# Performance work log

Hardware: AMD Instinct MI355X
Metric: run time of the kernel (lower is better)

## Reference

```python
import jax, jax.numpy as jnp
import numpy as np

N_, E_, A_, B_, H_, DH_ = 8000, 12000, 48000, 64, 64, 4096
STEPS, POOL_ITERS = 4, 3

def rbf(x, K, cutoff):
    mu = jnp.linspace(0.0, cutoff, K).astype(x.dtype)
    gamma = 1.0 / (cutoff / (K - 1)) ** 2
    return jnp.exp(-gamma * (x[..., None] - mu) ** 2)

def gru_step(x, h, Wih, Whh, bih, bhh):
    gi = x @ Wih.T + bih
    gh = h @ Whh.T + bhh
    ir, iz, inew = jnp.split(gi, 3, axis=-1)
    hr, hz, hnew = jnp.split(gh, 3, axis=-1)
    r = jax.nn.sigmoid(ir + hr)
    z = jax.nn.sigmoid(iz + hz)
    n = jnp.tanh(inew + r * hnew)
    return (1.0 - z) * n + z * h

def lstm_step(x, h, c, Wih, Whh, bih, bhh):
    g = x @ Wih.T + bih + h @ Whh.T + bhh
    i, f, gg, o = jnp.split(g, 4, axis=-1)
    c2 = jax.nn.sigmoid(f) * c + jax.nn.sigmoid(i) * jnp.tanh(gg)
    h2 = jax.nn.sigmoid(o) * jnp.tanh(c2)
    return h2, c2

def seg_softmax(e, seg, num_seg):
    m = jax.ops.segment_max(e, seg, num_segments=num_seg)
    ex = jnp.exp(e - m[seg])
    s = jax.ops.segment_sum(ex, seg, num_segments=num_seg)
    return ex / s[seg]

def _forward(node_attribute, edge_attribute, edge_length, angle, edge_src, edge_dst, angle_src, angle_dst, graph_ids, projW, projb, bondW, bondb, efW, efb, gnn_b, buW, bub, auW, aub, gWih, gWhh, gbih, gbhh, sWih0, sWhh0, sbih0, sbhh0, sWih1, sWhh1, sbih1, sbhh1, spW, spb, prelu_a):
    N, E = node_attribute.shape[0], edge_src.shape[0]
    x0 = jax.nn.relu(node_attribute @ projW + projb)  # [N, H]
    len_rbf = rbf(edge_length, 8, 4.0)                # [E, 8]
    edge_feat = jnp.concatenate([edge_attribute, len_rbf], axis=-1)  # [E, 16]
    ee_feat = jnp.concatenate([rbf(angle, 8, float(np.pi)), len_rbf[angle_src]], axis=-1)  # [A, 16]
    Wb = (edge_feat @ bondW + bondb).reshape(E, H_, H_)  # per-bond weight matrices (constant over steps)
    Wa = (ee_feat @ efW + efb).reshape(-1, H_, H_)       # per-angle weight matrices
    nf, hid = x0, x0
    for _ in range(STEPS):
        bm = nf[edge_src]                                # gather src node feats per bond [E, H]
        ha = jax.nn.relu(bm @ auW + aub)                 # angle_update
        m_ang = jnp.einsum('ai,aio->ao', ha[angle_src], Wa)  # [A, H]
        amsg = jax.ops.segment_sum(m_ang, angle_dst, num_segments=E)  # scatter-sum to bonds
        hb = jax.nn.relu(bm @ buW + bub) + amsg          # bond_update + angle message
        m = jnp.einsum('ei,eio->eo', hb, Wb)             # [E, H]
        nf = jax.nn.relu(jax.ops.segment_sum(m, edge_dst, num_segments=N) + gnn_b)
        nf = gru_step(nf, hid, gWih, gWhh, gbih, gbhh)   # 1-step, 1-layer GRU: output == new hidden
        hid = nf
    agg = jnp.concatenate([nf, x0], axis=-1)             # [N, 2H]
    D = agg.shape[-1]
    q_star = jnp.zeros((B_, 2 * D), agg.dtype)
    h0 = jnp.zeros((B_, D), agg.dtype); c0 = h0
    h1 = h0; c1 = h0
    for _ in range(POOL_ITERS):                          # Set2Set
        h0, c0 = lstm_step(q_star, h0, c0, sWih0, sWhh0, sbih0, sbhh0)
        h1, c1 = lstm_step(h0, h1, c1, sWih1, sWhh1, sbih1, sbhh1)
        q = h1                                           # [B, D]
        e = jnp.sum(agg * q[graph_ids], axis=-1)         # [N]
        alpha = seg_softmax(e, graph_ids, B_)
        readout = jax.ops.segment_sum(alpha[:, None] * agg, graph_ids, num_segments=B_)
        q_star = jnp.concatenate([q, readout], axis=-1)  # [B, 2D]
    out = q_star @ spW + spb                             # [B, DH]
    return jnp.where(out >= 0, out, prelu_a * out)       # PReLU

def setup_inputs():
    key = jax.random.key(0)
    ks = jax.random.split(key, 40)
    r = lambda i, shape, s=1.0: s * jax.random.normal(ks[i], shape, jnp.float32)
    inp = {}
    inp['node_attribute'] = r(0, (N_, 110))
    inp['edge_attribute'] = r(1, (E_, 8))
    inp['edge_length'] = jax.random.uniform(ks[2], (E_,), jnp.float32, 0.5, 4.0)
    inp['angle'] = jax.random.uniform(ks[3], (A_,), jnp.float32, 0.0, float(np.pi))
    inp['edge_src'] = jax.random.randint(ks[4], (E_,), 0, N_)
    inp['edge_dst'] = jax.random.randint(ks[5], (E_,), 0, N_)
    inp['angle_src'] = jax.random.randint(ks[6], (A_,), 0, E_)
    inp['angle_dst'] = jax.random.randint(ks[7], (A_,), 0, E_)
    inp['graph_ids'] = jnp.sort(jax.random.randint(ks[8], (N_,), 0, B_))
    w = 0.05
    inp['projW'] = r(9, (110, H_), w); inp['projb'] = jnp.zeros((H_,), jnp.float32)
    inp['bondW'] = r(10, (16, H_ * H_), w); inp['bondb'] = jnp.zeros((H_ * H_,), jnp.float32)
    inp['efW'] = r(11, (16, H_ * H_), w); inp['efb'] = jnp.zeros((H_ * H_,), jnp.float32)
    inp['gnn_b'] = jnp.zeros((H_,), jnp.float32)
    inp['buW'] = r(12, (H_, H_), w); inp['bub'] = jnp.zeros((H_,), jnp.float32)
    inp['auW'] = r(13, (H_, H_), w); inp['aub'] = jnp.zeros((H_,), jnp.float32)
    inp['gWih'] = r(14, (3 * H_, H_), w); inp['gWhh'] = r(15, (3 * H_, H_), w)
    inp['gbih'] = jnp.zeros((3 * H_,), jnp.float32); inp['gbhh'] = jnp.zeros((3 * H_,), jnp.float32)
    D = 2 * H_  # Set2Set feature dim = 128
    inp['sWih0'] = r(16, (4 * D, 2 * D), w); inp['sWhh0'] = r(17, (4 * D, D), w)
    inp['sbih0'] = jnp.zeros((4 * D,), jnp.float32); inp['sbhh0'] = jnp.zeros((4 * D,), jnp.float32)
    inp['sWih1'] = r(18, (4 * D, D), w); inp['sWhh1'] = r(19, (4 * D, D), w)
    inp['sbih1'] = jnp.zeros((4 * D,), jnp.float32); inp['sbhh1'] = jnp.zeros((4 * D,), jnp.float32)
    inp['spW'] = r(20, (4 * H_, DH_), w); inp['spb'] = jnp.zeros((DH_,), jnp.float32)
    inp['prelu_a'] = jnp.full((1,), 0.25, jnp.float32)
    return inp

def reference(node_attribute, edge_attribute, edge_length, angle, edge_src, edge_dst, angle_src, angle_dst, graph_ids, projW, projb, bondW, bondb, efW, efb, gnn_b, buW, bub, auW, aub, gWih, gWhh, gbih, gbhh, sWih0, sWhh0, sbih0, sbhh0, sWih1, sWhh1, sbih1, sbhh1, spW, spb, prelu_a):
    return _forward(node_attribute, edge_attribute, edge_length, angle, edge_src, edge_dst, angle_src, angle_dst, graph_ids, projW, projb, bondW, bondb, efW, efb, gnn_b, buW, bub, auW, aub, gWih, gWhh, gbih, gbhh, sWih0, sWhh0, sbih0, sbhh0, sWih1, sWhh1, sbih1, sbhh1, spW, spb, prelu_a)
```

## Files before the change

kernel.cpp:

```cpp
#include <hip/hip_runtime.h>
#include <math.h>

#define N_N 8000
#define N_E 12000
#define N_A 48000
#define N_B 64
#define N_H 64
#define N_DH 4096

typedef _Float16 h16;
typedef __attribute__((ext_vector_type(8))) _Float16 h16x8;
typedef __attribute__((ext_vector_type(4))) float f32x4;

__device__ __forceinline__ float atomAddF(float* p, float v) {
  return __hip_atomic_fetch_add(p, v, __ATOMIC_RELAXED, __HIP_MEMORY_SCOPE_AGENT);
}
__device__ __forceinline__ float sigm(float x) { return 1.f / (1.f + expf(-x)); }


__global__ void k_proj(const float* __restrict__ na, const float* __restrict__ W,
                       const float* __restrict__ b, float* __restrict__ x0) {
  int wid = (blockIdx.x * blockDim.x + threadIdx.x) >> 6;
  int lane = threadIdx.x & 63;
  if (wid >= N_N) return;
  const float* row = na + (size_t)wid * 110;
  float acc = b[lane];
  for (int k = 0; k < 110; ++k) acc = fmaf(row[k], W[k * 64 + lane], acc);
  x0[(size_t)wid * 64 + lane] = fmaxf(acc, 0.f);
}

__global__ void k_feat(const float* __restrict__ ea, const float* __restrict__ el,
                       const float* __restrict__ ang, const int* __restrict__ asrc,
                       float* __restrict__ ef, float* __restrict__ ee) {
  int i = blockIdx.x * blockDim.x + threadIdx.x;
  const float g2 = (7.f / 4.f) * (7.f / 4.f);
  if (i < N_E) {
    int e = i;
    float x = el[e];
#pragma unroll
    for (int j = 0; j < 8; ++j) ef[e * 16 + j] = ea[e * 8 + j];
#pragma unroll
    for (int j = 0; j < 8; ++j) {
      float d = x - j * (4.f / 7.f);
      ef[e * 16 + 8 + j] = expf(-g2 * d * d);
    }
  } else if (i < N_E + N_A) {
    int a = i - N_E;
    const float PIf = 3.14159265358979323846f;
    float x = ang[a];
    float g1 = (7.f / PIf) * (7.f / PIf);
#pragma unroll
    for (int j = 0; j < 8; ++j) {
      float d = x - j * (PIf / 7.f);
      ee[a * 16 + j] = expf(-g1 * d * d);
    }
    float y = el[asrc[a]];
#pragma unroll
    for (int j = 0; j < 8; ++j) {
      float d = y - j * (4.f / 7.f);
      ee[a * 16 + 8 + j] = expf(-g2 * d * d);
    }
  }
}

#define PREP_B0 32768
#define PREP_B1 (PREP_B0 + 69632)
#define PREP_B2 (PREP_B1 + 69632)
#define PREP_B3 (PREP_B2 + 4096)
#define PREP_B4 (PREP_B3 + 4096)
__global__ void k_prep(const float* __restrict__ gWih, const float* __restrict__ gWhh,
                       const float* __restrict__ efW, const float* __restrict__ efb,
                       const float* __restrict__ bondW, const float* __restrict__ bondb,
                       const float* __restrict__ auW, const float* __restrict__ buW,
                       h16* __restrict__ W3t, h16* __restrict__ ttA,
                       h16* __restrict__ ttB, h16* __restrict__ wtAU,
                       h16* __restrict__ wtBU) {
  int i = blockIdx.x * blockDim.x + threadIdx.x;
  if (i < PREP_B0) {
    int col = i >> 7, k = i & 127;
    int grp = col >> 6, u = col & 63;
    float v;
    if (grp == 0) v = (k < 64) ? gWih[u * 64 + k] : gWhh[u * 64 + k - 64];
    else if (grp == 1) v = (k < 64) ? gWih[(64 + u) * 64 + k] : gWhh[(64 + u) * 64 + k - 64];
    else if (grp == 2) v = (k < 64) ? gWih[(128 + u) * 64 + k] : 0.f;
    else v = (k < 64) ? 0.f : gWhh[(128 + u) * 64 + k - 64];
    W3t[i] = (h16)v;
  } else if (i < PREP_B1) {
    int j = i - PREP_B0;
    int n = j >> 6, i2 = j & 63;
    int k = n >> 6, o = n & 63;
    float val = (k < 16) ? efW[(size_t)k * 4096 + i2 * 64 + o] : efb[i2 * 64 + o];
    ttA[j] = (h16)val;
  } else if (i < PREP_B2) {
    int j = i - PREP_B1;
    int n = j >> 6, i2 = j & 63;
    int k = n >> 6, o = n & 63;
    float val = (k < 16) ? bondW[(size_t)k * 4096 + i2 * 64 + o] : bondb[i2 * 64 + o];
    ttB[j] = (h16)val;
  } else if (i < PREP_B3) {
    int j = i - PREP_B2;
    int o = j >> 6, i2 = j & 63;
    wtAU[j] = (h16)auW[i2 * 64 + o];
  } else if (i < PREP_B4) {
    int j = i - PREP_B3;
    int o = j >> 6, i2 = j & 63;
    wtBU[j] = (h16)buW[i2 * 64 + o];
  }
}

__global__ void k_bounds2(const int* __restrict__ gid, int* __restrict__ gstart,
                          int* __restrict__ gend) {
  int n = blockIdx.x * blockDim.x + threadIdx.x;
  if (n >= N_N) return;
  int g = gid[n];
  if (n == 0 || gid[n - 1] != g) gstart[g] = n;
  if (n == N_N - 1 || gid[n + 1] != g) gend[g] = n + 1;
}


template <bool ADD_AMSG>
__global__ __launch_bounds__(256) void k_mfma_mlp(
    const float* __restrict__ v, const int* __restrict__ src,
    const h16* __restrict__ Wt, const float* __restrict__ bias,
    const float* __restrict__ amsg, h16* __restrict__ out, int T,
    float4* __restrict__ zbuf, int zcount4) {
  if (blockIdx.y == 0 && zbuf) {
    int stride = gridDim.x * 256;
    for (int i = blockIdx.x * 256 + threadIdx.x; i < zcount4; i += stride)
      zbuf[i] = (float4){0.f, 0.f, 0.f, 0.f};
  }
  int tid = threadIdx.x, wave = tid >> 6, lane = tid & 63;
  int l15 = lane & 15, lq = lane >> 4;
  int oc = blockIdx.y;
  int ib0 = blockIdx.x * 128 + wave * 32;

  h16x8 afr[2][2];
#pragma unroll
  for (int s = 0; s < 2; ++s) {
    int item = ib0 + s * 16 + l15;
    if (item >= T) item = T - 1;
    const float* vp = v + (size_t)src[item] * 64;
#pragma unroll
    for (int ks = 0; ks < 2; ++ks) {
      const float4* p = (const float4*)(vp + ks * 32 + 8 * lq);
      float4 x0 = p[0], x1 = p[1];
      h16x8 a;
      a[0] = (h16)x0.x; a[1] = (h16)x0.y; a[2] = (h16)x0.z; a[3] = (h16)x0.w;
      a[4] = (h16)x1.x; a[5] = (h16)x1.y; a[6] = (h16)x1.z; a[7] = (h16)x1.w;
      afr[s][ks] = a;
    }
  }
  h16x8 bfr[2][2];
#pragma unroll
  for (int nt = 0; nt < 2; ++nt)
#pragma unroll
    for (int ks = 0; ks < 2; ++ks)
      bfr[nt][ks] = *(const h16x8*)(Wt + (size_t)((oc * 2 + nt) * 16 + l15) * 64 +
                                    ks * 32 + 8 * lq);

  f32x4 acc[2][2];
#pragma unroll
  for (int s = 0; s < 2; ++s)
#pragma unroll
    for (int nt = 0; nt < 2; ++nt) acc[s][nt] = (f32x4){0.f, 0.f, 0.f, 0.f};
#pragma unroll
  for (int s = 0; s < 2; ++s)
#pragma unroll
    for (int nt = 0; nt < 2; ++nt)
#pragma unroll
      for (int ks = 0; ks < 2; ++ks)
        acc[s][nt] = __builtin_amdgcn_mfma_f32_16x16x32_f16(afr[s][ks], bfr[nt][ks],
                                                            acc[s][nt], 0, 0, 0);
#pragma unroll
  for (int s = 0; s < 2; ++s) {
#pragma unroll
    for (int nt = 0; nt < 2; ++nt) {
      int o = (oc * 2 + nt) * 16 + l15;
      float bo = bias[o];
#pragma unroll
      for (int r = 0; r < 4; ++r) {
        int item = ib0 + s * 16 + lq * 4 + r;
        if (item < T) {
          float val = fmaxf(acc[s][nt][r] + bo, 0.f);
          if (ADD_AMSG) val += amsg[(size_t)item * 64 + o];
          out[(size_t)item * 64 + o] = (h16)val;
        }
      }
    }
  }
}

template <bool GATHER>
__global__ __launch_bounds__(256) void k_mfma_mm(
    const h16* __restrict__ v, const int* __restrict__ src,
    const float* __restrict__ feat, const h16* __restrict__ Tt,
    const int* __restrict__ dst, float* __restrict__ out, int T) {
  __shared__ float f_lds[128 * 17];
  __shared__ int dst_lds[128];
  int tid = threadIdx.x;
  int base = blockIdx.x * 128;
  int oc = blockIdx.y;
  for (int e = tid; e < 128 * 16; e += 256) {
    int il = e >> 4, k = e & 15;
    int g = base + il;
    if (g >= T) g = T - 1;
    f_lds[il * 17 + k] = feat[(size_t)g * 16 + k];
  }
  if (tid < 128) {
    int g = base + tid;
    if (g >= T) g = T - 1;
    dst_lds[tid] = dst[g];
  }
  __syncthreads();

  int wave = tid >> 6, lane = tid & 63;
  int l15 = lane & 15, lq = lane >> 4;
  int ibl = wave * 32;
  int ib0 = base + ibl;

  h16x8 afr[2][2];
#pragma unroll
  for (int s = 0; s < 2; ++s) {
    int item = ib0 + s * 16 + l15;
    if (item >= T) item = T - 1;
    int vi = GATHER ? src[item] : item;
    const h16* vp = v + (size_t)vi * 64;
#pragma unroll
    for (int ks = 0; ks < 2; ++ks)
      afr[s][ks] = *(const h16x8*)(vp + ks * 32 + 8 * lq);
  }

  f32x4 acc[2][2];
#pragma unroll
  for (int s = 0; s < 2; ++s)
#pragma unroll
    for (int nt = 0; nt < 2; ++nt) acc[s][nt] = (f32x4){0.f, 0.f, 0.f, 0.f};

  for (int kk = 0; kk < 16; ++kk) {
    h16x8 bfr[2][2];
#pragma unroll
    for (int nt = 0; nt < 2; ++nt)
#pragma unroll
      for (int ks = 0; ks < 2; ++ks)
        bfr[nt][ks] = *(const h16x8*)(Tt + (size_t)(kk * 64 + (oc * 2 + nt) * 16 + l15) * 64 +
                                      ks * 32 + 8 * lq);
    h16x8 a2[2][2];
#pragma unroll
    for (int s = 0; s < 2; ++s) {
      h16 fs = (h16)f_lds[(ibl + s * 16 + l15) * 17 + kk];
      a2[s][0] = afr[s][0] * fs;
      a2[s][1] = afr[s][1] * fs;
    }
#pragma unroll
    for (int s = 0; s < 2; ++s)
#pragma unroll
      for (int nt = 0; nt < 2; ++nt)
#pragma unroll
        for (int ks = 0; ks < 2; ++ks)
          acc[s][nt] = __builtin_amdgcn_mfma_f32_16x16x32_f16(a2[s][ks], bfr[nt][ks],
                                                              acc[s][nt], 0, 0, 0);
  }
  {
    h16x8 bfr[2][2];
#pragma unroll
    for (int nt = 0; nt < 2; ++nt)
#pragma unroll
      for (int ks = 0; ks < 2; ++ks)
        bfr[nt][ks] = *(const h16x8*)(Tt + (size_t)(16 * 64 + (oc * 2 + nt) * 16 + l15) * 64 +
                                      ks * 32 + 8 * lq);
#pragma unroll
    for (int s = 0; s < 2; ++s)
#pragma unroll
      for (int nt = 0; nt < 2; ++nt)
#pragma unroll
        for (int ks = 0; ks < 2; ++ks)
          acc[s][nt] = __builtin_amdgcn_mfma_f32_16x16x32_f16(afr[s][ks], bfr[nt][ks],
                                                              acc[s][nt], 0, 0, 0);
  }

#pragma unroll
  for (int s = 0; s < 2; ++s) {
#pragma unroll
    for (int r = 0; r < 4; ++r) {
      int il = ibl + s * 16 + lq * 4 + r;
      int item = base + il;
      if (item < T) {
        float* op = out + (size_t)dst_lds[il] * 64;
#pragma unroll
        for (int nt = 0; nt < 2; ++nt)
          atomAddF(op + (oc * 2 + nt) * 16 + l15, acc[s][nt][r]);
      }
    }
  }
}

__global__ __launch_bounds__(256) void k_gru2(
    const float* __restrict__ nacc, const float* __restrict__ gnnb,
    const float* __restrict__ h, const h16* __restrict__ W3t,
    const float* __restrict__ gbih, const float* __restrict__ gbhh,
    float* __restrict__ hout, const float* __restrict__ x0,
    float* __restrict__ agg, int wagg) {
  int tid = threadIdx.x, wave = tid >> 6, lane = tid & 63;
  int l15 = lane & 15, lq = lane >> 4;
  int ib0 = blockIdx.x * 64 + wave * 16;
  int nodeA = ib0 + l15;
  if (nodeA >= N_N) nodeA = N_N - 1;

  h16x8 afr[4];
#pragma unroll
  for (int ks = 0; ks < 2; ++ks) {
    const float4* p = (const float4*)(nacc + (size_t)nodeA * 64 + ks * 32 + 8 * lq);
    const float4* gp = (const float4*)(gnnb + ks * 32 + 8 * lq);
    float4 v0 = p[0], v1 = p[1], g0 = gp[0], g1 = gp[1];
    h16x8 a;
    a[0] = (h16)fmaxf(v0.x + g0.x, 0.f); a[1] = (h16)fmaxf(v0.y + g0.y, 0.f);
    a[2] = (h16)fmaxf(v0.z + g0.z, 0.f); a[3] = (h16)fmaxf(v0.w + g0.w, 0.f);
    a[4] = (h16)fmaxf(v1.x + g1.x, 0.f); a[5] = (h16)fmaxf(v1.y + g1.y, 0.f);
    a[6] = (h16)fmaxf(v1.z + g1.z, 0.f); a[7] = (h16)fmaxf(v1.w + g1.w, 0.f);
    afr[ks] = a;
  }
#pragma unroll
  for (int ks = 0; ks < 2; ++ks) {
    const float4* p = (const float4*)(h + (size_t)nodeA * 64 + ks * 32 + 8 * lq);
    float4 v0 = p[0], v1 = p[1];
    h16x8 a;
    a[0] = (h16)v0.x; a[1] = (h16)v0.y; a[2] = (h16)v0.z; a[3] = (h16)v0.w;
    a[4] = (h16)v1.x; a[5] = (h16)v1.y; a[6] = (h16)v1.z; a[7] = (h16)v1.w;
    afr[2 + ks] = a;
  }

  f32x4 acc[16];
#pragma unroll
  for (int nt = 0; nt < 16; ++nt) acc[nt] = (f32x4){0.f, 0.f, 0.f, 0.f};
#pragma unroll
  for (int nt = 0; nt < 16; ++nt) {
#pragma unroll
    for (int ks = 0; ks < 4; ++ks) {
      if (nt >= 8 && nt < 12 && ks >= 2) continue;
      if (nt >= 12 && ks < 2) continue;
      h16x8 b = *(const h16x8*)(W3t + (size_t)(nt * 16 + l15) * 128 + ks * 32 + 8 * lq);
      acc[nt] = __builtin_amdgcn_mfma_f32_16x16x32_f16(afr[ks], b, acc[nt], 0, 0, 0);
    }
  }

#pragma unroll
  for (int nt0 = 0; nt0 < 4; ++nt0) {
    int u = nt0 * 16 + l15;
    float br = gbih[u] + gbhh[u];
    float bz = gbih[64 + u] + gbhh[64 + u];
    float bin_ = gbih[128 + u];
    float bhn = gbhh[128 + u];
#pragma unroll
    for (int r = 0; r < 4; ++r) {
      int node = ib0 + lq * 4 + r;
      if (node < N_N) {
        float rr = sigm(acc[nt0][r] + br);
        float zz = sigm(acc[nt0 + 4][r] + bz);
        float nn = tanhf(acc[nt0 + 8][r] + bin_ + rr * (acc[nt0 + 12][r] + bhn));
        float hv = h[(size_t)node * 64 + u];
        float val = (1.f - zz) * nn + zz * hv;
        hout[(size_t)node * 64 + u] = val;
        if (wagg) {
          agg[(size_t)node * 128 + u] = val;
          agg[(size_t)node * 128 + 64 + u] = x0[(size_t)node * 64 + u];
        }
      }
    }
  }
}


__global__ __launch_bounds__(256) void k_lstm2(
    const float* __restrict__ x, int xdim,
    const float* __restrict__ hin, const float* __restrict__ cin,
    const float* __restrict__ Wih, const float* __restrict__ Whh,
    const float* __restrict__ bih, const float* __restrict__ bhh,
    float* __restrict__ hout, float* __restrict__ cout) {
  int w = (blockIdx.x * blockDim.x + threadIdx.x) >> 6;
  int lane = threadIdx.x & 63;
  if (w >= N_B * 128) return;
  int b = w >> 7, u = w & 127;
  float a0 = 0.f, a1 = 0.f, a2 = 0.f, a3 = 0.f;
  const float* xr = x + (size_t)b * xdim;
  for (int k = lane; k < xdim; k += 64) {
    float xv = xr[k];
    a0 = fmaf(xv, Wih[(size_t)u * xdim + k], a0);
    a1 = fmaf(xv, Wih[(size_t)(128 + u) * xdim + k], a1);
    a2 = fmaf(xv, Wih[(size_t)(256 + u) * xdim + k], a2);
    a3 = fmaf(xv, Wih[(size_t)(384 + u) * xdim + k], a3);
  }
  const float* hr = hin + (size_t)b * 128;
#pragma unroll
  for (int k0 = 0; k0 < 128; k0 += 64) {
    int k = k0 + lane;
    float hv = hr[k];
    a0 = fmaf(hv, Whh[(size_t)u * 128 + k], a0);
    a1 = fmaf(hv, Whh[(size_t)(128 + u) * 128 + k], a1);
    a2 = fmaf(hv, Whh[(size_t)(256 + u) * 128 + k], a2);
    a3 = fmaf(hv, Whh[(size_t)(384 + u) * 128 + k], a3);
  }
#pragma unroll
  for (int m = 1; m < 64; m <<= 1) {
    a0 += __shfl_xor(a0, m);
    a1 += __shfl_xor(a1, m);
    a2 += __shfl_xor(a2, m);
    a3 += __shfl_xor(a3, m);
  }
  if (lane == 0) {
    float gi = a0 + bih[u] + bhh[u];
    float gf = a1 + bih[128 + u] + bhh[128 + u];
    float gg = a2 + bih[256 + u] + bhh[256 + u];
    float go = a3 + bih[384 + u] + bhh[384 + u];
    float c2 = sigm(gf) * cin[(size_t)b * 128 + u] + sigm(gi) * tanhf(gg);
    hout[(size_t)b * 128 + u] = sigm(go) * tanhf(c2);
    cout[(size_t)b * 128 + u] = c2;
  }
}

__global__ __launch_bounds__(256) void k_pool2(
    const float* __restrict__ agg, const int* __restrict__ gstart,
    const int* __restrict__ gend, const float* __restrict__ q,
    float* __restrict__ q_star) {
  int g = blockIdx.x;
  int s = gstart[g], t = gend[g];
  int cnt = t - s;
  if (cnt < 0) cnt = 0;
  if (cnt > 1024) cnt = 1024;
  __shared__ float ew[1024];
  __shared__ float red[8];
  __shared__ float comb[256];
  int tid = threadIdx.x, wave = tid >> 6, lane = tid & 63;
  float qa = q[g * 128 + lane], qb = q[g * 128 + 64 + lane];
  for (int i = wave; i < cnt; i += 4) {
    int n = s + i;
    float a = agg[(size_t)n * 128 + lane] * qa + agg[(size_t)n * 128 + 64 + lane] * qb;
#pragma unroll
    for (int m = 1; m < 64; m <<= 1) a += __shfl_xor(a, m);
    if (lane == 0) ew[i] = a;
  }
  __syncthreads();
  float mx = -INFINITY;
  for (int i = tid; i < cnt; i += 256) mx = fmaxf(mx, ew[i]);
#pragma unroll
  for (int m = 1; m < 64; m <<= 1) mx = fmaxf(mx, __shfl_xor(mx, m));
  if (lane == 0) red[wave] = mx;
  __syncthreads();
  mx = fmaxf(fmaxf(red[0], red[1]), fmaxf(red[2], red[3]));
  float sm = 0.f;
  for (int i = tid; i < cnt; i += 256) sm += expf(ew[i] - mx);
#pragma unroll
  for (int m = 1; m < 64; m <<= 1) sm += __shfl_xor(sm, m);
  if (lane == 0) red[4 + wave] = sm;
  __syncthreads();
  sm = red[4] + red[5] + red[6] + red[7];
  float inv = (sm > 0.f) ? 1.f / sm : 0.f;
  __syncthreads();
  for (int i = tid; i < cnt; i += 256) ew[i] = expf(ew[i] - mx) * inv;
  __syncthreads();
  int d = tid & 127, half = tid >> 7;
  float acc = 0.f;
  for (int i = half; i < cnt; i += 2)
    acc = fmaf(ew[i], agg[(size_t)(s + i) * 128 + d], acc);
  comb[tid] = acc;
  __syncthreads();
  if (half == 0) {
    float r2 = acc + comb[128 + tid];
    q_star[(size_t)g * 256 + d] = q[(size_t)g * 128 + d];
    q_star[(size_t)g * 256 + 128 + d] = r2;
  }
}

__global__ void k_out(const float* __restrict__ qs, const float* __restrict__ W,
                      const float* __restrict__ bias, const float* __restrict__ pa,
                      float* __restrict__ out) {
  int idx = blockIdx.x * blockDim.x + threadIdx.x;
  if (idx >= N_B * N_DH) return;
  int b = idx >> 12, d = idx & 4095;
  float acc = bias[d];
  const float* q = qs + (size_t)b * 256;
  for (int k = 0; k < 256; ++k) acc = fmaf(q[k], W[(size_t)k * 4096 + d], acc);
  float a = pa[0];
  out[idx] = acc >= 0.f ? acc : a * acc;
}

enum : size_t {
  OFF_X0 = 0,
  OFF_HA = OFF_X0 + (size_t)N_N * 64,
  OFF_HB = OFF_HA + (size_t)N_N * 64,
  OFF_EF = OFF_HB + (size_t)N_N * 64,
  OFF_EE = OFF_EF + (size_t)N_E * 16,
  OFF_HAE = OFF_EE + (size_t)N_A * 16,
  OFF_AMSG = OFF_HAE + (size_t)N_E * 64,
  OFF_HBE = OFF_AMSG + (size_t)N_E * 64,
  OFF_NACC = OFF_HBE + (size_t)N_E * 64,
  OFF_AGG = OFF_NACC + (size_t)N_N * 64,
  OFF_QSTAR = OFF_AGG + (size_t)N_N * 128,
  OFF_H0A = OFF_QSTAR + N_B * 256,
  OFF_H0B = OFF_H0A + N_B * 128,
  OFF_C0A = OFF_H0B + N_B * 128,
  OFF_C0B = OFF_C0A + N_B * 128,
  OFF_H1A = OFF_C0B + N_B * 128,
  OFF_H1B = OFF_H1A + N_B * 128,
  OFF_C1A = OFF_H1B + N_B * 128,
  OFF_C1B = OFF_C1A + N_B * 128,
  OFF_GSTART = OFF_C1B + N_B * 128,
  OFF_GEND = OFF_GSTART + N_B,
  OFF_TT_ANG = (OFF_GEND + N_B + 63) & ~(size_t)63,
  OFF_TT_BOND = OFF_TT_ANG + 34816,
  OFF_WT_AU = OFF_TT_BOND + 34816,
  OFF_WT_BU = OFF_WT_AU + 2048,
  OFF_W3T = OFF_WT_BU + 2048,
  WS_FLOATS = OFF_W3T + 16384
};

extern "C" void kernel_launch(void* const* d_in, const int* in_sizes, int n_in,
                              void* d_out, int out_size, void* d_ws, size_t ws_size,
                              hipStream_t stream) {
  (void)in_sizes; (void)n_in; (void)out_size; (void)ws_size;
  const float* na    = (const float*)d_in[0];
  const float* ea    = (const float*)d_in[1];
  const float* el    = (const float*)d_in[2];
  const float* ang   = (const float*)d_in[3];
  const int*   esrc  = (const int*)d_in[4];
  const int*   edst  = (const int*)d_in[5];
  const int*   asrc  = (const int*)d_in[6];
  const int*   adst  = (const int*)d_in[7];
  const int*   gid   = (const int*)d_in[8];
  const float* projW = (const float*)d_in[9];
  const float* projb = (const float*)d_in[10];
  const float* bondW = (const float*)d_in[11];
  const float* bondb = (const float*)d_in[12];
  const float* efW   = (const float*)d_in[13];
  const float* efb   = (const float*)d_in[14];
  const float* gnnb  = (const float*)d_in[15];
  const float* buW   = (const float*)d_in[16];
  const float* bub   = (const float*)d_in[17];
  const float* auW   = (const float*)d_in[18];
  const float* aub   = (const float*)d_in[19];
  const float* gWih  = (const float*)d_in[20];
  const float* gWhh  = (const float*)d_in[21];
  const float* gbih  = (const float*)d_in[22];
  const float* gbhh  = (const float*)d_in[23];
  const float* sWih0 = (const float*)d_in[24];
  const float* sWhh0 = (const float*)d_in[25];
  const float* sbih0 = (const float*)d_in[26];
  const float* sbhh0 = (const float*)d_in[27];
  const float* sWih1 = (const float*)d_in[28];
  const float* sWhh1 = (const float*)d_in[29];
  const float* sbih1 = (const float*)d_in[30];
  const float* sbhh1 = (const float*)d_in[31];
  const float* spW   = (const float*)d_in[32];
  const float* spb   = (const float*)d_in[33];
  const float* pa    = (const float*)d_in[34];
  float* out = (float*)d_out;
  float* ws = (float*)d_ws;

  float* x0   = ws + OFF_X0;
  float* hA   = ws + OFF_HA;
  float* hB   = ws + OFF_HB;
  float* ef   = ws + OFF_EF;
  float* ee   = ws + OFF_EE;
  h16*   ha_h = (h16*)(ws + OFF_HAE);
  float* amsg = ws + OFF_AMSG;
  h16*   hb_h = (h16*)(ws + OFF_HBE);
  float* nacc = ws + OFF_NACC;
  float* agg  = ws + OFF_AGG;
  float* qstar = ws + OFF_QSTAR;
  float* h0a = ws + OFF_H0A; float* h0b = ws + OFF_H0B;
  float* c0a = ws + OFF_C0A; float* c0b = ws + OFF_C0B;
  float* h1a = ws + OFF_H1A; float* h1b = ws + OFF_H1B;
  float* c1a = ws + OFF_C1A; float* c1b = ws + OFF_C1B;
  int* gstart = (int*)(ws + OFF_GSTART);
  int* gend   = (int*)(ws + OFF_GEND);
  h16* ttA = (h16*)(ws + OFF_TT_ANG);
  h16* ttB = (h16*)(ws + OFF_TT_BOND);
  h16* wtAU = (h16*)(ws + OFF_WT_AU);
  h16* wtBU = (h16*)(ws + OFF_WT_BU);
  h16* w3t  = (h16*)(ws + OFF_W3T);

  k_proj<<<(N_N * 64 + 255) / 256, 256, 0, stream>>>(na, projW, projb, x0);
  k_feat<<<(N_E + N_A + 255) / 256, 256, 0, stream>>>(ea, el, ang, asrc, ef, ee);
  k_prep<<<(PREP_B4 + 255) / 256, 256, 0, stream>>>(gWih, gWhh, efW, efb, bondW,
                                                    bondb, auW, buW, w3t, ttA, ttB,
                                                    wtAU, wtBU);
  hipMemsetAsync(gstart, 0x7f, N_B * sizeof(int), stream);
  hipMemsetAsync(gend, 0, N_B * sizeof(int), stream);
  k_bounds2<<<(N_N + 255) / 256, 256, 0, stream>>>(gid, gstart, gend);

  const int MLP_GX = (N_E + 127) / 128;
  const float* cur = x0;
  float* bufs[2] = {hA, hB};
  for (int s = 0; s < 4; ++s) {
    k_mfma_mlp<false><<<dim3(MLP_GX, 2), 256, 0, stream>>>(
        cur, esrc, wtAU, aub, nullptr, ha_h, N_E, (float4*)amsg, N_E * 64 / 4);
    k_mfma_mm<true><<<dim3((N_A + 127) / 128, 2), 256, 0, stream>>>(
        ha_h, asrc, ee, ttA, adst, amsg, N_A);
    k_mfma_mlp<true><<<dim3(MLP_GX, 2), 256, 0, stream>>>(
        cur, esrc, wtBU, bub, amsg, hb_h, N_E, (float4*)nacc, N_N * 64 / 4);
    k_mfma_mm<false><<<dim3(MLP_GX, 2), 256, 0, stream>>>(
        hb_h, nullptr, ef, ttB, edst, nacc, N_E);
    float* nxt = bufs[s & 1];
    k_gru2<<<(N_N + 63) / 64, 256, 0, stream>>>(nacc, gnnb, cur, w3t, gbih, gbhh,
                                                nxt, x0, agg, (s == 3) ? 1 : 0);
    cur = nxt;
  }

  hipMemsetAsync(qstar, 0, (size_t)(N_B * 256 + 8 * N_B * 128) * sizeof(float), stream);
  float *h0i = h0a, *h0o = h0b, *c0i = c0a, *c0o = c0b;
  float *h1i = h1a, *h1o = h1b, *c1i = c1a, *c1o = c1b;
  for (int it = 0; it < 3; ++it) {
    k_lstm2<<<(N_B * 128 * 64 + 255) / 256, 256, 0, stream>>>(
        qstar, 256, h0i, c0i, sWih0, sWhh0, sbih0, sbhh0, h0o, c0o);
    k_lstm2<<<(N_B * 128 * 64 + 255) / 256, 256, 0, stream>>>(
        h0o, 128, h1i, c1i, sWih1, sWhh1, sbih1, sbhh1, h1o, c1o);
    k_pool2<<<N_B, 256, 0, stream>>>(agg, gstart, gend, h1o, qstar);
    float* tmp;
    tmp = h0i; h0i = h0o; h0o = tmp;
    tmp = c0i; c0i = c0o; c0o = tmp;
    tmp = h1i; h1i = h1o; h1o = tmp;
    tmp = c1i; c1i = c1o; c1o = tmp;
  }
  k_out<<<(N_B * N_DH + 255) / 256, 256, 0, stream>>>(qstar, spW, spb, pa, out);
}
```

Baseline: 460.0 us.

## Fuse edge MLPs into message matmuls and merge setup kernels into one

```diff
diff --git a/kernel.cpp b/kernel.cpp
--- a/kernel.cpp
+++ b/kernel.cpp
@@ -17,184 +17,134 @@
 }
 __device__ __forceinline__ float sigm(float x) { return 1.f / (1.f + expf(-x)); }
 
-
-__global__ void k_proj(const float* __restrict__ na, const float* __restrict__ W,
-                       const float* __restrict__ b, float* __restrict__ x0) {
-  int wid = (blockIdx.x * blockDim.x + threadIdx.x) >> 6;
-  int lane = threadIdx.x & 63;
-  if (wid >= N_N) return;
-  const float* row = na + (size_t)wid * 110;
-  float acc = b[lane];
-  for (int k = 0; k < 110; ++k) acc = fmaf(row[k], W[k * 64 + lane], acc);
-  x0[(size_t)wid * 64 + lane] = fmaxf(acc, 0.f);
-}
-
-__global__ void k_feat(const float* __restrict__ ea, const float* __restrict__ el,
-                       const float* __restrict__ ang, const int* __restrict__ asrc,
-                       float* __restrict__ ef, float* __restrict__ ee) {
-  int i = blockIdx.x * blockDim.x + threadIdx.x;
-  const float g2 = (7.f / 4.f) * (7.f / 4.f);
-  if (i < N_E) {
-    int e = i;
-    float x = el[e];
-#pragma unroll
-    for (int j = 0; j < 8; ++j) ef[e * 16 + j] = ea[e * 8 + j];
-#pragma unroll
-    for (int j = 0; j < 8; ++j) {
-      float d = x - j * (4.f / 7.f);
-      ef[e * 16 + 8 + j] = expf(-g2 * d * d);
-    }
-  } else if (i < N_E + N_A) {
-    int a = i - N_E;
-    const float PIf = 3.14159265358979323846f;
-    float x = ang[a];
-    float g1 = (7.f / PIf) * (7.f / PIf);
-#pragma unroll
-    for (int j = 0; j < 8; ++j) {
-      float d = x - j * (PIf / 7.f);
-      ee[a * 16 + j] = expf(-g1 * d * d);
-    }
-    float y = el[asrc[a]];
-#pragma unroll
-    for (int j = 0; j < 8; ++j) {
-      float d = y - j * (4.f / 7.f);
-      ee[a * 16 + 8 + j] = expf(-g2 * d * d);
-    }
-  }
-}
-
+#define SB_PROJ 2000
+#define SB_FEAT (SB_PROJ + 235)
+#define SB_PREP (SB_FEAT + 704)
+#define SB_BND  (SB_PREP + 32)
+#define SB_ZERO (SB_BND + 1330)
 #define PREP_B0 32768
 #define PREP_B1 (PREP_B0 + 69632)
 #define PREP_B2 (PREP_B1 + 69632)
 #define PREP_B3 (PREP_B2 + 4096)
 #define PREP_B4 (PREP_B3 + 4096)
-__global__ void k_prep(const float* __restrict__ gWih, const float* __restrict__ gWhh,
-                       const float* __restrict__ efW, const float* __restrict__ efb,
-                       const float* __restrict__ bondW, const float* __restrict__ bondb,
-                       const float* __restrict__ auW, const float* __restrict__ buW,
-                       h16* __restrict__ W3t, h16* __restrict__ ttA,
-                       h16* __restrict__ ttB, h16* __restrict__ wtAU,
-                       h16* __restrict__ wtBU) {
-  int i = blockIdx.x * blockDim.x + threadIdx.x;
-  if (i < PREP_B0) {
-    int col = i >> 7, k = i & 127;
-    int grp = col >> 6, u = col & 63;
-    float v;
-    if (grp == 0) v = (k < 64) ? gWih[u * 64 + k] : gWhh[u * 64 + k - 64];
-    else if (grp == 1) v = (k < 64) ? gWih[(64 + u) * 64 + k] : gWhh[(64 + u) * 64 + k - 64];
-    else if (grp == 2) v = (k < 64) ? gWih[(128 + u) * 64 + k] : 0.f;
-    else v = (k < 64) ? 0.f : gWhh[(128 + u) * 64 + k - 64];
-    W3t[i] = (h16)v;
-  } else if (i < PREP_B1) {
-    int j = i - PREP_B0;
-    int n = j >> 6, i2 = j & 63;
-    int k = n >> 6, o = n & 63;
-    float val = (k < 16) ? efW[(size_t)k * 4096 + i2 * 64 + o] : efb[i2 * 64 + o];
-    ttA[j] = (h16)val;
-  } else if (i < PREP_B2) {
-    int j = i - PREP_B1;
-    int n = j >> 6, i2 = j & 63;
-    int k = n >> 6, o = n & 63;
-    float val = (k < 16) ? bondW[(size_t)k * 4096 + i2 * 64 + o] : bondb[i2 * 64 + o];
-    ttB[j] = (h16)val;
-  } else if (i < PREP_B3) {
-    int j = i - PREP_B2;
-    int o = j >> 6, i2 = j & 63;
-    wtAU[j] = (h16)auW[i2 * 64 + o];
-  } else if (i < PREP_B4) {
-    int j = i - PREP_B3;
-    int o = j >> 6, i2 = j & 63;
-    wtBU[j] = (h16)buW[i2 * 64 + o];
-  }
-}
-
-__global__ void k_bounds2(const int* __restrict__ gid, int* __restrict__ gstart,
-                          int* __restrict__ gend) {
-  int n = blockIdx.x * blockDim.x + threadIdx.x;
-  if (n >= N_N) return;
-  int g = gid[n];
-  if (n == 0 || gid[n - 1] != g) gstart[g] = n;
-  if (n == N_N - 1 || gid[n + 1] != g) gend[g] = n + 1;
-}
-
-
-template <bool ADD_AMSG>
-__global__ __launch_bounds__(256) void k_mfma_mlp(
-    const float* __restrict__ v, const int* __restrict__ src,
-    const h16* __restrict__ Wt, const float* __restrict__ bias,
-    const float* __restrict__ amsg, h16* __restrict__ out, int T,
+
+__global__ __launch_bounds__(256) void k_setup(
+    const float* __restrict__ na, const float* __restrict__ projW,
+    const float* __restrict__ projb, const float* __restrict__ ea,
+    const float* __restrict__ el, const float* __restrict__ ang,
+    const int* __restrict__ asrc, const int* __restrict__ gid,
+    const float* __restrict__ gWih, const float* __restrict__ gWhh,
+    const float* __restrict__ efW, const float* __restrict__ efb,
+    const float* __restrict__ bondW, const float* __restrict__ bondb,
+    const float* __restrict__ auW, const float* __restrict__ buW,
+    float* __restrict__ x0, float* __restrict__ ef, float* __restrict__ ee,
+    int* __restrict__ gstart, int* __restrict__ gend,
+    h16* __restrict__ W3t, h16* __restrict__ ttA, h16* __restrict__ ttB,
+    h16* __restrict__ wtAU, h16* __restrict__ wtBU,
+    float4* __restrict__ amsg0_4, float4* __restrict__ nacc0_4,
+    float4* __restrict__ qz_4) {
+  int bx = blockIdx.x, tid = threadIdx.x;
+  if (bx < SB_PROJ) {
+    int wid = bx * 4 + (tid >> 6);
+    int lane = tid & 63;
+    if (wid < N_N) {
+      const float* row = na + (size_t)wid * 110;
+      float acc = projb[lane];
+      for (int k = 0; k < 110; ++k) acc = fmaf(row[k], projW[k * 64 + lane], acc);
+      x0[(size_t)wid * 64 + lane] = fmaxf(acc, 0.f);
+    }
+  } else if (bx < SB_FEAT) {
+    int i = (bx - SB_PROJ) * 256 + tid;
+    const float g2 = (7.f / 4.f) * (7.f / 4.f);
+    if (i < N_E) {
+      int e = i;
+      float x = el[e];
+#pragma unroll
+      for (int j = 0; j < 8; ++j) ef[e * 16 + j] = ea[e * 8 + j];
+#pragma unroll
+      for (int j = 0; j < 8; ++j) {
+        float d = x - j * (4.f / 7.f);
+        ef[e * 16 + 8 + j] = expf(-g2 * d * d);
+      }
+    } else if (i < N_E + N_A) {
+      int a = i - N_E;
+      const float PIf = 3.14159265358979323846f;
+      float x = ang[a];
+      float g1 = (7.f / PIf) * (7.f / PIf);
+#pragma unroll
+      for (int j = 0; j < 8; ++j) {
+        float d = x - j * (PIf / 7.f);
+        ee[a * 16 + j] = expf(-g1 * d * d);
+      }
+      float y = el[asrc[a]];
+#pragma unroll
+      for (int j = 0; j < 8; ++j) {
+        float d = y - j * (4.f / 7.f);
+        ee[a * 16 + 8 + j] = expf(-g2 * d * d);
+      }
+    }
+  } else if (bx < SB_PREP) {
+    int i = (bx - SB_FEAT) * 256 + tid;
+    if (i < PREP_B0) {
+      int col = i >> 7, k = i & 127;
+      int grp = col >> 6, u = col & 63;
+      float v;
+      if (grp == 0) v = (k < 64) ? gWih[u * 64 + k] : gWhh[u * 64 + k - 64];
+      else if (grp == 1) v = (k < 64) ? gWih[(64 + u) * 64 + k] : gWhh[(64 + u) * 64 + k - 64];
+      else if (grp == 2) v = (k < 64) ? gWih[(128 + u) * 64 + k] : 0.f;
+      else v = (k < 64) ? 0.f : gWhh[(128 + u) * 64 + k - 64];
+      W3t[i] = (h16)v;
+    } else if (i < PREP_B1) {
+      int j = i - PREP_B0;
+      int n = j >> 6, i2 = j & 63;
+      int k = n >> 6, o = n & 63;
+      float val = (k < 16) ? efW[(size_t)k * 4096 + i2 * 64 + o] : efb[i2 * 64 + o];
+      ttA[j] = (h16)val;
+    } else if (i < PREP_B2) {
+      int j = i - PREP_B1;
+      int n = j >> 6, i2 = j & 63;
+      int k = n >> 6, o = n & 63;
+      float val = (k < 16) ? bondW[(size_t)k * 4096 + i2 * 64 + o] : bondb[i2 * 64 + o];
+      ttB[j] = (h16)val;
+    } else if (i < PREP_B3) {
+      int j = i - PREP_B2;
+      int o = j >> 6, i2 = j & 63;
+      wtAU[j] = (h16)auW[i2 * 64 + o];
+    } else if (i < PREP_B4) {
+      int j = i - PREP_B3;
+      int o = j >> 6, i2 = j & 63;
+      wtBU[j] = (h16)buW[i2 * 64 + o];
+    }
+  } else if (bx < SB_BND) {
+    int n = (bx - SB_PREP) * 256 + tid;
+    if (n < N_N) {
+      int g = gid[n];
+      if (n == 0 || gid[n - 1] != g) gstart[g] = n;
+      if (n == N_N - 1 || gid[n + 1] != g) gend[g] = n + 1;
+    }
+  } else if (bx < SB_ZERO) {
+    int i = (bx - SB_BND) * 256 + tid;
+    float4 z = (float4){0.f, 0.f, 0.f, 0.f};
+    if (i < 192000) amsg0_4[i] = z;
+    else if (i < 320000) nacc0_4[i - 192000] = z;
+    else if (i < 340480) qz_4[i - 320000] = z;
+  }
+}
+
+template <bool ANGLE>
+__global__ __launch_bounds__(256) void k_fused_mm(
+    const float* __restrict__ xcur, const int* __restrict__ map,
+    const int* __restrict__ esrc, const h16* __restrict__ WtU,
+    const float* __restrict__ biasU, const float* __restrict__ amsg_in,
+    const float* __restrict__ feat, const h16* __restrict__ Tt,
+    const int* __restrict__ dst, float* __restrict__ outacc, int T,
     float4* __restrict__ zbuf, int zcount4) {
-  if (blockIdx.y == 0 && zbuf) {
+  if (zbuf && blockIdx.y == 0) {
     int stride = gridDim.x * 256;
     for (int i = blockIdx.x * 256 + threadIdx.x; i < zcount4; i += stride)
       zbuf[i] = (float4){0.f, 0.f, 0.f, 0.f};
   }
-  int tid = threadIdx.x, wave = tid >> 6, lane = tid & 63;
-  int l15 = lane & 15, lq = lane >> 4;
-  int oc = blockIdx.y;
-  int ib0 = blockIdx.x * 128 + wave * 32;
-
-  h16x8 afr[2][2];
-#pragma unroll
-  for (int s = 0; s < 2; ++s) {
-    int item = ib0 + s * 16 + l15;
-    if (item >= T) item = T - 1;
-    const float* vp = v + (size_t)src[item] * 64;
-#pragma unroll
-    for (int ks = 0; ks < 2; ++ks) {
-      const float4* p = (const float4*)(vp + ks * 32 + 8 * lq);
-      float4 x0 = p[0], x1 = p[1];
-      h16x8 a;
-      a[0] = (h16)x0.x; a[1] = (h16)x0.y; a[2] = (h16)x0.z; a[3] = (h16)x0.w;
-      a[4] = (h16)x1.x; a[5] = (h16)x1.y; a[6] = (h16)x1.z; a[7] = (h16)x1.w;
-      afr[s][ks] = a;
-    }
-  }
-  h16x8 bfr[2][2];
-#pragma unroll
-  for (int nt = 0; nt < 2; ++nt)
-#pragma unroll
-    for (int ks = 0; ks < 2; ++ks)
-      bfr[nt][ks] = *(const h16x8*)(Wt + (size_t)((oc * 2 + nt) * 16 + l15) * 64 +
-                                    ks * 32 + 8 * lq);
-
-  f32x4 acc[2][2];
-#pragma unroll
-  for (int s = 0; s < 2; ++s)
-#pragma unroll
-    for (int nt = 0; nt < 2; ++nt) acc[s][nt] = (f32x4){0.f, 0.f, 0.f, 0.f};
-#pragma unroll
-  for (int s = 0; s < 2; ++s)
-#pragma unroll
-    for (int nt = 0; nt < 2; ++nt)
-#pragma unroll
-      for (int ks = 0; ks < 2; ++ks)
-        acc[s][nt] = __builtin_amdgcn_mfma_f32_16x16x32_f16(afr[s][ks], bfr[nt][ks],
-                                                            acc[s][nt], 0, 0, 0);
-#pragma unroll
-  for (int s = 0; s < 2; ++s) {
-#pragma unroll
-    for (int nt = 0; nt < 2; ++nt) {
-      int o = (oc * 2 + nt) * 16 + l15;
-      float bo = bias[o];
-#pragma unroll
-      for (int r = 0; r < 4; ++r) {
-        int item = ib0 + s * 16 + lq * 4 + r;
-        if (item < T) {
-          float val = fmaxf(acc[s][nt][r] + bo, 0.f);
-          if (ADD_AMSG) val += amsg[(size_t)item * 64 + o];
-          out[(size_t)item * 64 + o] = (h16)val;
-        }
-      }
-    }
-  }
-}
-
-template <bool GATHER>
-__global__ __launch_bounds__(256) void k_mfma_mm(
-    const h16* __restrict__ v, const int* __restrict__ src,
-    const float* __restrict__ feat, const h16* __restrict__ Tt,
-    const int* __restrict__ dst, float* __restrict__ out, int T) {
+  __shared__ h16 haT[4][2048];
   __shared__ float f_lds[128 * 17];
   __shared__ int dst_lds[128];
   int tid = threadIdx.x;
@@ -217,17 +167,72 @@
   int l15 = lane & 15, lq = lane >> 4;
   int ibl = wave * 32;
   int ib0 = base + ibl;
+  h16* myT = haT[wave];
+
+  {
+    h16x8 xafr[2][2];
+#pragma unroll
+    for (int s = 0; s < 2; ++s) {
+      int item = ib0 + s * 16 + l15;
+      if (item >= T) item = T - 1;
+      int e = ANGLE ? map[item] : item;
+      const float* vp = xcur + (size_t)esrc[e] * 64;
+#pragma unroll
+      for (int ks = 0; ks < 2; ++ks) {
+        const float4* p = (const float4*)(vp + ks * 32 + 8 * lq);
+        float4 v0 = p[0], v1 = p[1];
+        h16x8 a;
+        a[0] = (h16)v0.x; a[1] = (h16)v0.y; a[2] = (h16)v0.z; a[3] = (h16)v0.w;
+        a[4] = (h16)v1.x; a[5] = (h16)v1.y; a[6] = (h16)v1.z; a[7] = (h16)v1.w;
+        xafr[s][ks] = a;
+      }
+    }
+    f32x4 aU[2][4];
+#pragma unroll
+    for (int s = 0; s < 2; ++s)
+#pragma unroll
+      for (int nt = 0; nt < 4; ++nt) aU[s][nt] = (f32x4){0.f, 0.f, 0.f, 0.f};
+#pragma unroll
+    for (int nt = 0; nt < 4; ++nt) {
+#pragma unroll
+      for (int ks = 0; ks < 2; ++ks) {
+        h16x8 b = *(const h16x8*)(WtU + (size_t)(nt * 16 + l15) * 64 + ks * 32 + 8 * lq);
+#pragma unroll
+        for (int s = 0; s < 2; ++s)
+          aU[s][nt] = __builtin_amdgcn_mfma_f32_16x16x32_f16(xafr[s][ks], b, aU[s][nt], 0, 0, 0);
+      }
+    }
+#pragma unroll
+    for (int s = 0; s < 2; ++s) {
+#pragma unroll
+      for (int nt = 0; nt < 4; ++nt) {
+        int o = nt * 16 + l15;
+        float bo = biasU[o];
+#pragma unroll
+        for (int r = 0; r < 4; ++r) {
+          int row = s * 16 + lq * 4 + r;
+          float val = fmaxf(aU[s][nt][r] + bo, 0.f);
+          if (!ANGLE) {
+            int item = ib0 + row;
+            if (item >= T) item = T - 1;
+            val += amsg_in[(size_t)item * 64 + o];
+          }
+          int idx = (((row * 64 + o) << 1) ^ ((row & 7) << 4)) >> 1;
+          myT[idx] = (h16)val;
+        }
+      }
+    }
+  }
 
   h16x8 afr[2][2];
 #pragma unroll
   for (int s = 0; s < 2; ++s) {
-    int item = ib0 + s * 16 + l15;
-    if (item >= T) item = T - 1;
-    int vi = GATHER ? src[item] : item;
-    const h16* vp = v + (size_t)vi * 64;
-#pragma unroll
-    for (int ks = 0; ks < 2; ++ks)
-      afr[s][ks] = *(const h16x8*)(vp + ks * 32 + 8 * lq);
+#pragma unroll
+    for (int ks = 0; ks < 2; ++ks) {
+      int row = s * 16 + l15;
+      int byte = ((row * 64 + ks * 32 + 8 * lq) << 1) ^ ((row & 7) << 4);
+      afr[s][ks] = *(const h16x8*)((const char*)myT + byte);
+    }
   }
 
   f32x4 acc[2][2];
@@ -285,7 +290,7 @@
       int il = ibl + s * 16 + lq * 4 + r;
       int item = base + il;
       if (item < T) {
-        float* op = out + (size_t)dst_lds[il] * 64;
+        float* op = outacc + (size_t)dst_lds[il] * 64;
 #pragma unroll
         for (int nt = 0; nt < 2; ++nt)
           atomAddF(op + (oc * 2 + nt) * 16 + l15, acc[s][nt][r]);
@@ -299,7 +304,12 @@
     const float* __restrict__ h, const h16* __restrict__ W3t,
     const float* __restrict__ gbih, const float* __restrict__ gbhh,
     float* __restrict__ hout, const float* __restrict__ x0,
-    float* __restrict__ agg, int wagg) {
+    float* __restrict__ agg, int wagg, float4* __restrict__ zbuf, int zcount4) {
+  if (zbuf) {
+    int stride = gridDim.x * 256;
+    for (int i = blockIdx.x * 256 + threadIdx.x; i < zcount4; i += stride)
+      zbuf[i] = (float4){0.f, 0.f, 0.f, 0.f};
+  }
   int tid = threadIdx.x, wave = tid >> 6, lane = tid & 63;
   int l15 = lane & 15, lq = lane >> 4;
   int ib0 = blockIdx.x * 64 + wave * 16;
@@ -489,11 +499,11 @@
   OFF_HB = OFF_HA + (size_t)N_N * 64,
   OFF_EF = OFF_HB + (size_t)N_N * 64,
   OFF_EE = OFF_EF + (size_t)N_E * 16,
-  OFF_HAE = OFF_EE + (size_t)N_A * 16,
-  OFF_AMSG = OFF_HAE + (size_t)N_E * 64,
-  OFF_HBE = OFF_AMSG + (size_t)N_E * 64,
-  OFF_NACC = OFF_HBE + (size_t)N_E * 64,
-  OFF_AGG = OFF_NACC + (size_t)N_N * 64,
+  OFF_AMSG0 = OFF_EE + (size_t)N_A * 16,
+  OFF_AMSG1 = OFF_AMSG0 + (size_t)N_E * 64,
+  OFF_NACC0 = OFF_AMSG1 + (size_t)N_E * 64,
+  OFF_NACC1 = OFF_NACC0 + (size_t)N_N * 64,
+  OFF_AGG = OFF_NACC1 + (size_t)N_N * 64,
   OFF_QSTAR = OFF_AGG + (size_t)N_N * 128,
   OFF_H0A = OFF_QSTAR + N_B * 256,
   OFF_H0B = OFF_H0A + N_B * 128,
@@ -555,57 +565,56 @@
   float* out = (float*)d_out;
   float* ws = (float*)d_ws;
 
-  float* x0   = ws + OFF_X0;
-  float* hA   = ws + OFF_HA;
-  float* hB   = ws + OFF_HB;
-  float* ef   = ws + OFF_EF;
-  float* ee   = ws + OFF_EE;
-  h16*   ha_h = (h16*)(ws + OFF_HAE);
-  float* amsg = ws + OFF_AMSG;
-  h16*   hb_h = (h16*)(ws + OFF_HBE);
-  float* nacc = ws + OFF_NACC;
-  float* agg  = ws + OFF_AGG;
+  float* x0    = ws + OFF_X0;
+  float* hA    = ws + OFF_HA;
+  float* hB    = ws + OFF_HB;
+  float* ef    = ws + OFF_EF;
+  float* ee    = ws + OFF_EE;
+  float* amsg0 = ws + OFF_AMSG0;
+  float* amsg1 = ws + OFF_AMSG1;
+  float* nacc0 = ws + OFF_NACC0;
+  float* nacc1 = ws + OFF_NACC1;
+  float* agg   = ws + OFF_AGG;
   float* qstar = ws + OFF_QSTAR;
   float* h0a = ws + OFF_H0A; float* h0b = ws + OFF_H0B;
   float* c0a = ws + OFF_C0A; float* c0b = ws + OFF_C0B;
   float* h1a = ws + OFF_H1A; float* h1b = ws + OFF_H1B;
   float* c1a = ws + OFF_C1A; float* c1b = ws + OFF_C1B;
   int* gstart = (int*)(ws + OFF_GSTART);
-  int* gend   = (int*)(ws + OFF_GEND);
   h16* ttA = (h16*)(ws + OFF_TT_ANG);
   h16* ttB = (h16*)(ws + OFF_TT_BOND);
   h16* wtAU = (h16*)(ws + OFF_WT_AU);
   h16* wtBU = (h16*)(ws + OFF_WT_BU);
   h16* w3t  = (h16*)(ws + OFF_W3T);
 
-  k_proj<<<(N_N * 64 + 255) / 256, 256, 0, stream>>>(na, projW, projb, x0);
-  k_feat<<<(N_E + N_A + 255) / 256, 256, 0, stream>>>(ea, el, ang, asrc, ef, ee);
-  k_prep<<<(PREP_B4 + 255) / 256, 256, 0, stream>>>(gWih, gWhh, efW, efb, bondW,
-                                                    bondb, auW, buW, w3t, ttA, ttB,
-                                                    wtAU, wtBU);
-  hipMemsetAsync(gstart, 0x7f, N_B * sizeof(int), stream);
-  hipMemsetAsync(gend, 0, N_B * sizeof(int), stream);
-  k_bounds2<<<(N_N + 255) / 256, 256, 0, stream>>>(gid, gstart, gend);
-
-  const int MLP_GX = (N_E + 127) / 128;
+  hipMemsetAsync(gstart, 0x7f, 2 * N_B * sizeof(int), stream);
+  k_setup<<<SB_ZERO, 256, 0, stream>>>(
+      na, projW, projb, ea, el, ang, asrc, gid, gWih, gWhh, efW, efb, bondW, bondb,
+      auW, buW, x0, ef, ee, gstart, gstart + N_B, w3t, ttA, ttB, wtAU, wtBU,
+      (float4*)amsg0, (float4*)nacc0, (float4*)qstar);
+
   const float* cur = x0;
   float* bufs[2] = {hA, hB};
+  float* amsgs[2] = {amsg0, amsg1};
+  float* naccs[2] = {nacc0, nacc1};
   for (int s = 0; s < 4; ++s) {
-    k_mfma_mlp<false><<<dim3(MLP_GX, 2), 256, 0, stream>>>(
-        cur, esrc, wtAU, aub, nullptr, ha_h, N_E, (float4*)amsg, N_E * 64 / 4);
-    k_mfma_mm<true><<<dim3((N_A + 127) / 128, 2), 256, 0, stream>>>(
-        ha_h, asrc, ee, ttA, adst, amsg, N_A);
-    k_mfma_mlp<true><<<dim3(MLP_GX, 2), 256, 0, stream>>>(
-        cur, esrc, wtBU, bub, amsg, hb_h, N_E, (float4*)nacc, N_N * 64 / 4);
-    k_mfma_mm<false><<<dim3(MLP_GX, 2), 256, 0, stream>>>(
-        hb_h, nullptr, ef, ttB, edst, nacc, N_E);
+    float* amsg_c = amsgs[s & 1];
+    float* amsg_o = amsgs[(s + 1) & 1];
+    float* nacc_c = naccs[s & 1];
+    float* nacc_o = naccs[(s + 1) & 1];
+    k_fused_mm<true><<<dim3((N_A + 127) / 128, 2), 256, 0, stream>>>(
+        cur, asrc, esrc, wtAU, aub, nullptr, ee, ttA, adst, amsg_c, N_A,
+        nullptr, 0);
+    k_fused_mm<false><<<dim3((N_E + 127) / 128, 2), 256, 0, stream>>>(
+        cur, nullptr, esrc, wtBU, bub, amsg_c, ef, ttB, edst, nacc_c, N_E,
+        (float4*)amsg_o, N_E * 64 / 4);
     float* nxt = bufs[s & 1];
-    k_gru2<<<(N_N + 63) / 64, 256, 0, stream>>>(nacc, gnnb, cur, w3t, gbih, gbhh,
-                                                nxt, x0, agg, (s == 3) ? 1 : 0);
+    k_gru2<<<(N_N + 63) / 64, 256, 0, stream>>>(nacc_c, gnnb, cur, w3t, gbih, gbhh,
+                                                nxt, x0, agg, (s == 3) ? 1 : 0,
+                                                (float4*)nacc_o, N_N * 64 / 4);
     cur = nxt;
   }
 
-  hipMemsetAsync(qstar, 0, (size_t)(N_B * 256 + 8 * N_B * 128) * sizeof(float), stream);
   float *h0i = h0a, *h0o = h0b, *c0i = c0a, *c0o = c0b;
   float *h1i = h1a, *h1o = h1b, *c1i = c1a, *c1o = c1b;
   for (int it = 0; it < 3; ++it) {
@@ -613,7 +622,7 @@
         qstar, 256, h0i, c0i, sWih0, sWhh0, sbih0, sbhh0, h0o, c0o);
     k_lstm2<<<(N_B * 128 * 64 + 255) / 256, 256, 0, stream>>>(
         h0o, 128, h1i, c1i, sWih1, sWhh1, sbih1, sbhh1, h1o, c1o);
-    k_pool2<<<N_B, 256, 0, stream>>>(agg, gstart, gend, h1o, qstar);
+    k_pool2<<<N_B, 256, 0, stream>>>(agg, gstart, gstart + N_B, h1o, qstar);
     float* tmp;
     tmp = h0i; h0i = h0o; h0o = tmp;
     tmp = c0i; c0i = c0o; c0o = tmp;
```

Result: faster. 414.4 us (-9.9%).
